# Performance work log

Measured on AMD Instinct MI355X. Metric: run time of the kernel, lower is better.

The kernel has to match this reference:

```python
import jax, jax.numpy as jnp
import numpy as np
import math

B, L, D = 2, 2048, 1024
H, HD = 16, 64          # num heads, head dim
R = 256                 # kv lora rank = D // 4
E, K, F = 8, 2, 1024    # routed experts, top_k, intermediate size


def rmsnorm(x, w, eps=1e-6):
    ms = jnp.mean(x * x, axis=-1, keepdims=True)
    return w * (x * jax.lax.rsqrt(ms + eps))


def setup_inputs() -> dict:
    key = jax.random.key(0)
    ks = jax.random.split(key, 16)
    s = 0.02
    return {
        "x": jax.random.normal(ks[0], (B, L, D), jnp.float32),
        "ln1_w": jnp.ones((D,), jnp.float32),
        "q_w": jax.random.normal(ks[1], (D, H * HD), jnp.float32) * s,
        "kvd_w": jax.random.normal(ks[2], (D, R), jnp.float32) * s,
        "kvn_w": jnp.ones((R,), jnp.float32),
        "kvu_w": jax.random.normal(ks[3], (R, 2 * H * HD), jnp.float32) * s,
        "o_w": jax.random.normal(ks[4], (H * HD, D), jnp.float32) * s,
        "ln2_w": jnp.ones((D,), jnp.float32),
        "gate_w": jax.random.normal(ks[5], (D, E), jnp.float32) * s,
        "sh_w1": jax.random.normal(ks[6], (D, F), jnp.float32) * s,
        "sh_w2": jax.random.normal(ks[7], (F, D), jnp.float32) * s,
        "sh_w3": jax.random.normal(ks[8], (D, F), jnp.float32) * s,
        "re_w1": jax.random.normal(ks[9], (E, D, F), jnp.float32) * s,
        "re_w2": jax.random.normal(ks[10], (E, F, D), jnp.float32) * s,
        "re_w3": jax.random.normal(ks[11], (E, D, F), jnp.float32) * s,
    }


def reference(x, ln1_w, q_w, kvd_w, kvn_w, kvu_w, o_w, ln2_w, gate_w,
              sh_w1, sh_w2, sh_w3, re_w1, re_w2, re_w3):
    # ---- MLHA attention with pre-RMSNorm and latent-compressed KV ----
    xn = rmsnorm(x, ln1_w)
    q = (xn @ q_w).reshape(B, L, H, HD)
    latent = rmsnorm(xn @ kvd_w, kvn_w)                 # [B,L,R]
    kv = latent @ kvu_w                                 # [B,L,2*H*HD]
    k, v = jnp.split(kv, 2, axis=-1)
    k = k.reshape(B, L, H, HD)
    v = v.reshape(B, L, H, HD)
    scores = jnp.einsum('bxhd,byhd->bhxy', q, k) / math.sqrt(HD)
    causal = jnp.tril(jnp.ones((L, L), bool))
    scores = jnp.where(causal, scores, -jnp.inf)
    attn = jax.nn.softmax(scores, axis=-1)
    attn_out = jnp.einsum('bhxy,byhd->bxhd', attn, v).reshape(B, L, H * HD)
    h = x + attn_out @ o_w

    # ---- MoE (inference: no jitter, expert_bias = 0, no bias update) ----
    hn = rmsnorm(h, ln2_w)
    flat = hn.reshape(-1, D)                            # [T,D], T=B*L
    # shared expert (SwiGLU)
    shared = (jax.nn.silu(flat @ sh_w1) * (flat @ sh_w3)) @ sh_w2
    # router
    logits = flat @ gate_w                              # [T,E]
    probs = jax.nn.softmax(logits, axis=-1)
    topw, topi = jax.lax.top_k(probs, K)                # [T,K]
    topw = topw / jnp.sum(topw, axis=-1, keepdims=True)
    # per-token per-expert combine weight [T,E]
    combine = jnp.sum(topw[..., None] * jax.nn.one_hot(topi, E, dtype=flat.dtype), axis=1)
    # all routed experts densely, then masked combine (same math as masked loop)
    h1 = jnp.einsum('td,edf->etf', flat, re_w1)
    h3 = jnp.einsum('td,edf->etf', flat, re_w3)
    eo = jnp.einsum('etf,efd->etd', jax.nn.silu(h1) * h3, re_w2)
    routed = jnp.einsum('te,etd->td', combine, eo)
    moe_out = (shared + routed).reshape(B, L, D)
    return h + moe_out, probs
```

## Files before the change

kernel.cpp:

```cpp
#include <hip/hip_runtime.h>
#include <hip/hip_bf16.h>
#include <cstdint>
#include <cstddef>

typedef unsigned short u16;
typedef unsigned int u32;
typedef __attribute__((ext_vector_type(8))) short bf16x8;
typedef __attribute__((ext_vector_type(4))) float f32x4;

static constexpr int Bb = 2, Ll = 2048, Dd = 1024, Hh = 16, Rr = 256, Ee = 8, Ff = 1024;
static constexpr int Tt = Bb * Ll;
static constexpr float QSCALE = 0.18033688011112042f;

__device__ __forceinline__ u16 f2bf(float f){
  union { float f; u32 u; } v; v.f = f;
  u32 u = v.u;
  u32 r = u + 0x7FFFu + ((u >> 16) & 1u);
  return (u16)(r >> 16);
}
__device__ __forceinline__ float bf2f(u16 b){
  union { u32 u; float f; } v; v.u = ((u32)b) << 16; return v.f;
}

#define GLDS(gp, lp) __builtin_amdgcn_global_load_lds( \
    (const __attribute__((address_space(1))) unsigned int*)(gp), \
    (__attribute__((address_space(3))) unsigned int*)(lp), 16, 0, 0)

__global__ void transpose5(const float* __restrict__ q_w, const float* __restrict__ o_w,
                           const float* __restrict__ w1, const float* __restrict__ w3,
                           const float* __restrict__ w2,
                           u16* __restrict__ qkvdT, u16* __restrict__ oT,
                           u16* __restrict__ sh13T, u16* __restrict__ sh2T){
  const float* s; u16* d; int off, str;
  switch (blockIdx.z){
    case 0: s = q_w; d = qkvdT; off = 0; str = 1; break;
    case 1: s = o_w; d = oT;    off = 0; str = 1; break;
    case 2: s = w1;  d = sh13T; off = 0; str = 2; break;
    case 3: s = w3;  d = sh13T; off = 1; str = 2; break;
    default: s = w2; d = sh2T;  off = 0; str = 1; break;
  }
  __shared__ float tile[32][33];
  int bx = blockIdx.x * 32, by = blockIdx.y * 32;
  int tx = threadIdx.x, ty = threadIdx.y;
  #pragma unroll
  for (int i = ty; i < 32; i += 8) tile[i][tx] = s[(size_t)(by + i) * 1024 + bx + tx];
  __syncthreads();
  #pragma unroll
  for (int i = ty; i < 32; i += 8)
    d[(size_t)(off + (bx + i) * str) * 1024 + by + tx] = f2bf(tile[tx][i]);
}

__global__ void transposeEx(const float* __restrict__ re_w1, const float* __restrict__ re_w3,
                            const float* __restrict__ re_w2,
                            u16* __restrict__ re13T, u16* __restrict__ re2T){
  int z = blockIdx.z, which = z >> 3, e = z & 7;
  const float* s; u16* d; int off, str;
  size_t eo = (size_t)e * 1024 * 1024;
  if (which == 0){ s = re_w1 + eo; d = re13T + (size_t)e * 2048 * 1024; off = 0; str = 2; }
  else if (which == 1){ s = re_w3 + eo; d = re13T + (size_t)e * 2048 * 1024; off = 1; str = 2; }
  else { s = re_w2 + eo; d = re2T + (size_t)e * 1024 * 1024; off = 0; str = 1; }
  __shared__ float tile[32][33];
  int bx = blockIdx.x * 32, by = blockIdx.y * 32;
  int tx = threadIdx.x, ty = threadIdx.y;
  #pragma unroll
  for (int i = ty; i < 32; i += 8) tile[i][tx] = s[(size_t)(by + i) * 1024 + bx + tx];
  __syncthreads();
  #pragma unroll
  for (int i = ty; i < 32; i += 8)
    d[(size_t)(off + (bx + i) * str) * 1024 + by + tx] = f2bf(tile[tx][i]);
}

__global__ void transpose_conv(const float* __restrict__ src, u16* __restrict__ dst,
                               int K, int N, int dstOff){
  __shared__ float tile[32][33];
  int bx = blockIdx.x * 32, by = blockIdx.y * 32;
  int tx = threadIdx.x, ty = threadIdx.y;
  #pragma unroll
  for (int i = ty; i < 32; i += 8) tile[i][tx] = src[(size_t)(by + i) * N + bx + tx];
  __syncthreads();
  #pragma unroll
  for (int i = ty; i < 32; i += 8)
    dst[(size_t)(dstOff + bx + i) * K + by + tx] = f2bf(tile[tx][i]);
}

template<int DIM>
__global__ void rmsnorm_kernel(const float* __restrict__ x, const float* __restrict__ w,
                               u16* __restrict__ out){
  int t = blockIdx.x;
  const float* xr = x + (size_t)t * DIM;
  u16* orow = out + (size_t)t * DIM;
  int tid = threadIdx.x;
  constexpr int NT = 256;
  constexpr int PER = DIM / NT > 0 ? DIM / NT : 1;
  float vals[PER];
  float ss = 0.f;
  #pragma unroll
  for (int i = 0; i < PER; i++){
    int d = tid + i * NT;
    float v = (d < DIM) ? xr[d] : 0.f;
    vals[i] = v; ss += v * v;
  }
  __shared__ float red[4];
  for (int m = 32; m; m >>= 1) ss += __shfl_xor(ss, m, 64);
  if ((tid & 63) == 0) red[tid >> 6] = ss;
  __syncthreads();
  float tot = red[0] + red[1] + red[2] + red[3];
  float rn = rsqrtf(tot / DIM + 1e-6f);
  #pragma unroll
  for (int i = 0; i < PER; i++){
    int d = tid + i * NT;
    if (d < DIM) orow[d] = f2bf(vals[i] * rn * w[d]);
  }
}

__global__ void router_kernel(const float* __restrict__ h, const float* __restrict__ ln2w,
                              const float* __restrict__ gate,
                              float* __restrict__ probs_out,
                              int* __restrict__ topi, float* __restrict__ topw,
                              u16* __restrict__ hn){
  int t = blockIdx.x; int tid = threadIdx.x;
  const float* hr = h + (size_t)t * Dd;
  float v[4]; float ss = 0.f;
  #pragma unroll
  for (int i = 0; i < 4; i++){ float x = hr[tid + i * 256]; v[i] = x; ss += x * x; }
  __shared__ float red[4];
  for (int m = 32; m; m >>= 1) ss += __shfl_xor(ss, m, 64);
  if ((tid & 63) == 0) red[tid >> 6] = ss;
  __syncthreads();
  float rn = rsqrtf((red[0] + red[1] + red[2] + red[3]) / Dd + 1e-6f);
  float p[8];
  #pragma unroll
  for (int e = 0; e < 8; e++) p[e] = 0.f;
  #pragma unroll
  for (int i = 0; i < 4; i++){
    int d = tid + i * 256;
    float hv = v[i] * rn * ln2w[d];
    hn[(size_t)t * Dd + d] = f2bf(hv);
    const float* g = gate + (size_t)d * 8;
    #pragma unroll
    for (int e = 0; e < 8; e++) p[e] += hv * g[e];
  }
  #pragma unroll
  for (int e = 0; e < 8; e++){
    float x = p[e];
    for (int m = 32; m; m >>= 1) x += __shfl_xor(x, m, 64);
    p[e] = x;
  }
  __shared__ float pe[4][8];
  if ((tid & 63) == 0){ for (int e = 0; e < 8; e++) pe[tid >> 6][e] = p[e]; }
  __syncthreads();
  if (tid == 0){
    float lg[8];
    for (int e = 0; e < 8; e++) lg[e] = pe[0][e] + pe[1][e] + pe[2][e] + pe[3][e];
    float mx = lg[0];
    for (int e = 1; e < 8; e++) mx = fmaxf(mx, lg[e]);
    float pr[8]; float s = 0.f;
    for (int e = 0; e < 8; e++){ pr[e] = __expf(lg[e] - mx); s += pr[e]; }
    float inv = 1.f / s;
    for (int e = 0; e < 8; e++) probs_out[(size_t)t * 8 + e] = pr[e] * inv;
    int i0 = 0;
    for (int e = 1; e < 8; e++) if (pr[e] > pr[i0]) i0 = e;
    int i1 = -1;
    for (int e = 0; e < 8; e++){ if (e == i0) continue; if (i1 < 0 || pr[e] > pr[i1]) i1 = e; }
    float w0 = pr[i0], w1 = pr[i1]; float wn = 1.f / (w0 + w1);
    topi[t * 2] = i0; topi[t * 2 + 1] = i1;
    topw[t * 2] = w0 * wn; topw[t * 2 + 1] = w1 * wn;
  }
}

__global__ void hist_kernel(const int* __restrict__ topi, int* __restrict__ counts){
  __shared__ int h[8];
  int tid = threadIdx.x;
  if (tid < 8) h[tid] = 0;
  __syncthreads();
  int base = blockIdx.x * 512;
  for (int i = tid; i < 512; i += 256) atomicAdd(&h[topi[base + i]], 1);
  __syncthreads();
  if (tid < 8) atomicAdd(&counts[tid], h[tid]);
}

__global__ void bucket_kernel(const int* __restrict__ topi, const float* __restrict__ topw,
                              const int* __restrict__ counts, int* __restrict__ cur,
                              int* __restrict__ entries, float* __restrict__ ew){
  __shared__ int lh[8], lbase[8], lcur[8], loffs[8];
  int tid = threadIdx.x;
  if (tid < 8) lh[tid] = 0;
  __syncthreads();
  int t = blockIdx.x * 256 + tid;
  int e0 = topi[t * 2], e1 = topi[t * 2 + 1];
  atomicAdd(&lh[e0], 1); atomicAdd(&lh[e1], 1);
  __syncthreads();
  if (tid == 0){
    int c = 0;
    for (int e = 0; e < 8; e++){ loffs[e] = c; c += counts[e]; }
  }
  if (tid < 8){ lbase[tid] = atomicAdd(&cur[tid], lh[tid]); lcur[tid] = 0; }
  __syncthreads();
  int p0 = atomicAdd(&lcur[e0], 1);
  int pos0 = loffs[e0] + lbase[e0] + p0;
  entries[pos0] = t; ew[pos0] = topw[t * 2];
  int p1 = atomicAdd(&lcur[e1], 1);
  int pos1 = loffs[e1] + lbase[e1] + p1;
  entries[pos1] = t; ew[pos1] = topw[t * 2 + 1];
}

template<int TM, int ROWMODE, int MODE>
__launch_bounds__(256)
__global__ void gemm_bt(const u16* __restrict__ A, const u16* __restrict__ Bt,
                        void* __restrict__ C, const float* __restrict__ res,
                        int M, int N, int K, int lda, int ldc,
                        const int* __restrict__ entries, const float* __restrict__ ew,
                        const int* __restrict__ counts,
                        float* __restrict__ outAt){
  constexpr int MTC = TM / 32;
  __shared__ __align__(16) u16 As[TM * 32];
  __shared__ __align__(16) u16 Bs[128 * 32];
  __shared__ int els[TM];
  __shared__ float ewl[TM];

  int e = (ROWMODE ? blockIdx.z : 0);
  const u16* Bte = Bt + (size_t)e * N * K;
  int cnt, off;
  if (ROWMODE == 0){ cnt = M; off = 0; }
  else {
    cnt = counts[e];
    off = 0;
    for (int i = 0; i < e; i++) off += counts[i];
  }
  int rt = blockIdx.y * TM;
  if (rt >= cnt) return;
  int cb = blockIdx.x * 128;
  int tid = threadIdx.x;

  if (ROWMODE >= 1){
    if (tid < TM){
      int r = rt + tid;
      els[tid] = (r < cnt) ? entries[off + r] : 0;
      ewl[tid] = (MODE == 4 && r < cnt) ? ew[off + r] : 0.f;
    }
    __syncthreads();
  }

  int sr = tid >> 2;
  int skc = (tid & 3) * 8;
  int rr0 = rt + sr, rr1 = rt + sr + 64;
  size_t ar0 = 0, ar1 = 0;
  if (ROWMODE == 0){ ar0 = (size_t)rr0; ar1 = (size_t)rr1; }
  else if (ROWMODE == 1){ ar0 = (size_t)els[sr];
                          ar1 = (TM == 128) ? (size_t)els[sr + 64] : 0; }
  else {
    int c0 = rr0 < cnt ? rr0 : (cnt - 1);
    int c1 = rr1 < cnt ? rr1 : (cnt - 1);
    ar0 = (size_t)off + c0; ar1 = (size_t)off + c1;
  }
  const u16* pa0 = A + ar0 * lda + skc;
  const u16* pa1 = A + ar1 * lda + skc;
  const u16* pb0 = Bte + (size_t)(cb + sr) * K + skc;
  const u16* pb1 = Bte + (size_t)(cb + sr + 64) * K + skc;
  u16* lA0 = &As[tid * 8];
  u16* lA1 = &As[(TM == 128 ? 2048 : 0) + tid * 8];
  u16* lB0 = &Bs[tid * 8];
  u16* lB1 = &Bs[2048 + tid * 8];

  int w = tid >> 6, lane = tid & 63;
  int wm = w >> 1, wn = w & 1;
  int quad = lane >> 4, l16 = lane & 15;

  f32x4 acc[MTC][4];
  const f32x4 zf = {0.f, 0.f, 0.f, 0.f};
  #pragma unroll
  for (int i = 0; i < MTC; i++)
    #pragma unroll
    for (int j = 0; j < 4; j++) acc[i][j] = zf;

  for (int k0 = 0; k0 < K; k0 += 32){
    __syncthreads();
    GLDS(pa0 + k0, lA0);
    if (TM == 128) GLDS(pa1 + k0, lA1);
    GLDS(pb0 + k0, lB0);
    GLDS(pb1 + k0, lB1);
    __syncthreads();
    bf16x8 af[MTC], bfr[4];
    #pragma unroll
    for (int mt = 0; mt < MTC; mt++)
      af[mt] = *(const bf16x8*)&As[(wm * (TM / 2) + mt * 16 + l16) * 32 + quad * 8];
    #pragma unroll
    for (int nt = 0; nt < 4; nt++)
      bfr[nt] = *(const bf16x8*)&Bs[(wn * 64 + nt * 16 + l16) * 32 + quad * 8];
    #pragma unroll
    for (int mt = 0; mt < MTC; mt++)
      #pragma unroll
      for (int nt = 0; nt < 4; nt++)
        acc[mt][nt] = __builtin_amdgcn_mfma_f32_16x16x32_bf16(af[mt], bfr[nt], acc[mt][nt], 0, 0, 0);
  }

  #pragma unroll
  for (int mt = 0; mt < MTC; mt++){
    #pragma unroll
    for (int nt = 0; nt < 4; nt++){
      #pragma unroll
      for (int r = 0; r < 4; r++){
        int row = wm * (TM / 2) + mt * 16 + quad * 4 + r;
        int col = cb + wn * 64 + nt * 16 + l16;
        int rr = rt + row;
        float v = acc[mt][nt][r];
        if (MODE == 6){
          float pv = __shfl_xor(v, 1, 64);
          if (rr < cnt && (l16 & 1) == 0){
            float sl = v / (1.f + __expf(-v));
            size_t crow = (size_t)((ROWMODE == 1) ? (off + rr) : rr);
            ((u16*)C)[crow * ldc + (col >> 1)] = f2bf(sl * pv);
          }
          continue;
        }
        if (rr >= cnt) continue;
        if (MODE == 0){
          size_t ci = (size_t)((ROWMODE == 1) ? (off + rr) : rr) * ldc + col;
          ((u16*)C)[ci] = f2bf(v);
        } else if (MODE == 1){
          size_t ci = (size_t)rr * ldc + col;
          ((float*)C)[ci] = v + res[ci];
        } else if (MODE == 5){
          if (col < 1024) ((u16*)C)[(size_t)rr * 1024 + col] = f2bf(v * QSCALE);
          else            outAt[(size_t)rr * 256 + (col - 1024)] = v;
        } else {
          int tok = els[row];
          atomicAdd(&outAt[(size_t)tok * ldc + col], ewl[row] * v);
        }
      }
    }
  }
}

#define RBAR() __builtin_amdgcn_s_barrier()
#define SBAR0() __builtin_amdgcn_sched_barrier(0)
#define VMCNT8() do{ asm volatile("s_waitcnt vmcnt(8)" ::: "memory"); \
                     __builtin_amdgcn_sched_barrier(0); }while(0)
#define VMCNT0() do{ asm volatile("s_waitcnt vmcnt(0)" ::: "memory"); \
                     __builtin_amdgcn_sched_barrier(0); }while(0)
#define MMQ(MQ, NQ, FA, FB) do{ \
  _Pragma("unroll") \
  for (int m4_ = 0; m4_ < 4; m4_++){ \
    _Pragma("unroll") \
    for (int n2_ = 0; n2_ < 2; n2_++){ \
      acc[(MQ)*4+m4_][(NQ)*2+n2_] = __builtin_amdgcn_mfma_f32_16x16x32_bf16(FA[m4_][0], FB[n2_][0], acc[(MQ)*4+m4_][(NQ)*2+n2_], 0, 0, 0); \
      acc[(MQ)*4+m4_][(NQ)*2+n2_] = __builtin_amdgcn_mfma_f32_16x16x32_bf16(FA[m4_][1], FB[n2_][1], acc[(MQ)*4+m4_][(NQ)*2+n2_], 0, 0, 0); \
    } \
  } }while(0)
#define RDA(DST, BB, MQ) do{ \
  _Pragma("unroll") \
  for (int m4_ = 0; m4_ < 4; m4_++){ \
    const char* p_ = (const char*)(&As[BB][0]) + (size_t)(wm*128 + (MQ)*64 + m4_*16 + l16)*128; \
    DST[m4_][0] = *(const bf16x8*)(p_ + offk0); \
    DST[m4_][1] = *(const bf16x8*)(p_ + offk1); \
  } }while(0)
#define RDB(DST, BB, NQ) do{ \
  _Pragma("unroll") \
  for (int n2_ = 0; n2_ < 2; n2_++){ \
    const char* p_ = (const char*)(&Bs[BB][0]) + (size_t)(wn*64 + (NQ)*32 + n2_*16 + l16)*128; \
    DST[n2_][0] = *(const bf16x8*)(p_ + offk0); \
    DST[n2_][1] = *(const bf16x8*)(p_ + offk1); \
  } }while(0)
#define STGA(SB, H, KT) do{ \
  GLDS(gA[(H)*2+0] + (size_t)(KT)*64, &As[SB][((H)*128 +  0)*64] + (size_t)tid*8); \
  GLDS(gA[(H)*2+1] + (size_t)(KT)*64, &As[SB][((H)*128 + 64)*64] + (size_t)tid*8); }while(0)
#define STGB(SB, H, KT) do{ \
  GLDS(gB[(H)*2+0] + (size_t)(KT)*64, &Bs[SB][((H)*128 +  0)*64] + (size_t)tid*8); \
  GLDS(gB[(H)*2+1] + (size_t)(KT)*64, &Bs[SB][((H)*128 + 64)*64] + (size_t)tid*8); }while(0)

__launch_bounds__(512, 2)
__global__ void gemm256_up(const u16* __restrict__ A,
                           const u16* __restrict__ sh13, const u16* __restrict__ re13,
                           u16* __restrict__ shg, u16* __restrict__ gr,
                           const int* __restrict__ entries, const int* __restrict__ counts){
  __shared__ __align__(16) u16 As[2][256 * 64];
  __shared__ __align__(16) u16 Bs[2][256 * 64];

  int e = blockIdx.z;
  int cnt, off = 0;
  if (e < 8){
    cnt = counts[e];
    for (int i = 0; i < e; i++) off += counts[i];
  } else cnt = Tt;
  int rt = blockIdx.y * 256;
  if (rt >= cnt) return;
  int cb = blockIdx.x * 256;
  const u16* Bte = (e < 8) ? (re13 + (size_t)e * 2048 * 1024) : sh13;
  u16* Cb = (e < 8) ? gr : shg;

  int tid = threadIdx.x;
  int w = tid >> 6, lane = tid & 63, quad = lane >> 4, l16 = lane & 15;
  int wm = w >> 2, wn = w & 3;
  int swz = (l16 & 7) << 4;
  int offk0 = (quad * 16) ^ swz;
  int offk1 = (64 + quad * 16) ^ swz;

  int trow = tid >> 3;
  int sk = ((((tid & 7) << 4) ^ ((trow & 7) << 4)) >> 1);
  const u16* gA[4]; const u16* gB[4];
  #pragma unroll
  for (int i = 0; i < 4; i++){
    int r = i * 64 + trow;
    int garow;
    if (e < 8){
      int idx = rt + r; if (idx >= cnt) idx = cnt - 1;
      garow = entries[off + idx];
    } else garow = rt + r;
    gA[i] = A + (size_t)garow * 1024 + sk;
    gB[i] = Bte + (size_t)(cb + r) * 1024 + sk;
  }

  f32x4 acc[8][4];
  const f32x4 zf = {0.f, 0.f, 0.f, 0.f};
  #pragma unroll
  for (int i = 0; i < 8; i++)
    #pragma unroll
    for (int j = 0; j < 4; j++) acc[i][j] = zf;

  auto tile = [&](int b, int t2, int mode){
    bf16x8 fa0[4][2], fa1[4][2], fb0[2][2], fb1[2][2];
    RDA(fa0, b, 0); RDB(fb0, b, 0);
    RDB(fb1, b, 1); RDA(fa1, b, 1);
    __builtin_amdgcn_s_setprio(1);
    MMQ(0, 0, fa0, fb0); MMQ(0, 1, fa0, fb1);
    MMQ(1, 0, fa1, fb0); MMQ(1, 1, fa1, fb1);
    __builtin_amdgcn_s_setprio(0);
    if (mode == 2) return;
    SBAR0();
    RBAR();
    if (mode == 0){
      STGB(b, 0, t2); STGB(b, 1, t2); STGA(b, 0, t2); STGA(b, 1, t2);
      VMCNT8();
    } else {
      VMCNT0();
    }
    RBAR();
    SBAR0();
  };

  STGB(0, 0, 0); STGB(0, 1, 0); STGA(0, 0, 0); STGA(0, 1, 0);
  STGB(1, 0, 1); STGB(1, 1, 1); STGA(1, 0, 1); STGA(1, 1, 1);
  VMCNT8();
  RBAR();

  for (int t = 0; t < 14; ++t) tile(t & 1, t + 2, 0);
  tile(0, 0, 1);
  tile(1, 0, 2);

  #pragma unroll
  for (int mi = 0; mi < 8; mi++){
    #pragma unroll
    for (int ni = 0; ni < 4; ni++){
      #pragma unroll
      for (int r = 0; r < 4; r++){
        int row = wm * 128 + (mi >> 2) * 64 + (mi & 3) * 16 + quad * 4 + r;
        int col = cb + wn * 64 + (ni >> 1) * 32 + (ni & 1) * 16 + l16;
        float v = acc[mi][ni][r];
        float pv = __shfl_xor(v, 1, 64);
        int grow = rt + row;
        if (grow < cnt && (l16 & 1) == 0){
          float sl = v / (1.f + __expf(-v));
          size_t crow = (e < 8) ? (size_t)(off + grow) : (size_t)grow;
          Cb[crow * 1024 + (col >> 1)] = f2bf(sl * pv);
        }
      }
    }
  }
}

__global__ void vt_kernel(const u16* __restrict__ kv, u16* __restrict__ vt){
  __shared__ __align__(16) u16 t[64 * 72];
  int kt = blockIdx.x * 64, h = blockIdx.y, b = blockIdx.z;
  size_t bL = (size_t)b * Ll;
  int tid = threadIdx.x;
  int r = tid >> 2, c0 = (tid & 3) * 16;
  const u16* src = kv + (bL + kt + r) * 2048 + 1024 + h * 64 + c0;
  *(uint4*)&t[r * 72 + c0]     = *(const uint4*)(src);
  *(uint4*)&t[r * 72 + c0 + 8] = *(const uint4*)(src + 8);
  __syncthreads();
  int d = tid >> 2; int k0 = (tid & 3) * 16;
  u16 tmp[16];
  #pragma unroll
  for (int j = 0; j < 16; j++) tmp[j] = t[(k0 + j) * 72 + d];
  u16* dst = vt + ((size_t)(b * Hh + h) * 64 + d) * (size_t)Ll + kt + k0;
  *(uint4*)dst       = *(const uint4*)&tmp[0];
  *(uint4*)(dst + 8) = *(const uint4*)&tmp[8];
}

__launch_bounds__(256)
__global__ void attn_kernel(const u16* __restrict__ q, const u16* __restrict__ kv,
                            const u16* __restrict__ vt, u16* __restrict__ out){
  constexpr int LD = 72;
  __shared__ __align__(16) u16 Ks[2][64 * LD];
  __shared__ __align__(16) u16 Vs[2][64 * LD];
  __shared__ __align__(16) u16 Ps[64 * LD];
  int h = blockIdx.y, b = blockIdx.z;
  size_t bL = (size_t)b * Ll;
  int tid = threadIdx.x, w = tid >> 6, lane = tid & 63, quad = lane >> 4, l16 = lane & 15;
  int sr = tid >> 2, sc = (tid & 3) * 16;
  const u16* kbase = kv + (bL + sr) * 2048 + h * 64 + sc;
  const u16* vbase = vt + ((size_t)(b * Hh + h) * 64 + sr) * (size_t)Ll + sc;
  const f32x4 zf = {0.f, 0.f, 0.f, 0.f};

  #pragma unroll
  for (int pass = 0; pass < 2; pass++){
    int q0 = (pass ? (31 - (int)blockIdx.x) : (int)blockIdx.x) * 64;
    int qrow = q0 + w * 16 + l16;

    bf16x8 qf[2];
    #pragma unroll
    for (int ks = 0; ks < 2; ks++)
      qf[ks] = *(const bf16x8*)(q + (bL + qrow) * 1024 + h * 64 + ks * 32 + quad * 8);

    f32x4 oacc[4];
    #pragma unroll
    for (int dt = 0; dt < 4; dt++) oacc[dt] = zf;
    float mprev = -1e30f, lsum = 0.f;

    uint4 kr0 = *(const uint4*)(kbase);
    uint4 kr1 = *(const uint4*)(kbase + 8);
    uint4 vr0 = *(const uint4*)(vbase);
    uint4 vr1 = *(const uint4*)(vbase + 8);
    *(uint4*)&Ks[0][sr * LD + sc]     = kr0;
    *(uint4*)&Ks[0][sr * LD + sc + 8] = kr1;
    *(uint4*)&Vs[0][sr * LD + sc]     = vr0;
    *(uint4*)&Vs[0][sr * LD + sc + 8] = vr1;
    int cur = 0;
    __syncthreads();

    for (int kt = 0; kt <= q0; kt += 64){
      bool pfetch = (kt + 64 <= q0);
      if (pfetch){
        const u16* kp = kbase + (size_t)(kt + 64) * 2048;
        kr0 = *(const uint4*)(kp);
        kr1 = *(const uint4*)(kp + 8);
        const u16* vp = vbase + kt + 64;
        vr0 = *(const uint4*)(vp);
        vr1 = *(const uint4*)(vp + 8);
      }
      const u16* ksp = Ks[cur];
      const u16* vsp = Vs[cur];

      f32x4 sacc[4];
      #pragma unroll
      for (int mt = 0; mt < 4; mt++) sacc[mt] = zf;
      __builtin_amdgcn_s_setprio(1);
      #pragma unroll
      for (int ks = 0; ks < 2; ks++){
        #pragma unroll
        for (int mt = 0; mt < 4; mt++){
          bf16x8 kf = *(const bf16x8*)&ksp[(mt * 16 + l16) * LD + ks * 32 + quad * 8];
          sacc[mt] = __builtin_amdgcn_mfma_f32_16x16x32_bf16(kf, qf[ks], sacc[mt], 0, 0, 0);
        }
      }
      __builtin_amdgcn_s_setprio(0);

      bool diag = (kt == q0);
      int lq = w * 16 + l16;
      float sv[16]; float mx = -1e30f;
      #pragma unroll
      for (int mt = 0; mt < 4; mt++){
        #pragma unroll
        for (int r = 0; r < 4; r++){
          float s = sacc[mt][r];
          if (diag && (mt * 16 + quad * 4 + r > lq)) s = -1e30f;
          sv[mt * 4 + r] = s;
          mx = fmaxf(mx, s);
        }
      }
      mx = fmaxf(mx, __shfl_xor(mx, 16, 64));
      mx = fmaxf(mx, __shfl_xor(mx, 32, 64));
      if (!__all(mx <= mprev)){
        float mnew = fmaxf(mprev, mx);
        float alpha = exp2f(mprev - mnew);
        mprev = mnew;
        lsum *= alpha;
        #pragma unroll
        for (int dt = 0; dt < 4; dt++) oacc[dt] *= alpha;
      }
      float rs = 0.f;
      #pragma unroll
      for (int mt = 0; mt < 4; mt++){
        float p0 = exp2f(sv[mt * 4 + 0] - mprev);
        float p1 = exp2f(sv[mt * 4 + 1] - mprev);
        float p2 = exp2f(sv[mt * 4 + 2] - mprev);
        float p3 = exp2f(sv[mt * 4 + 3] - mprev);
        rs += p0 + p1 + p2 + p3;
        union { uint2 u; __hip_bfloat162 h2[2]; } pk;
        pk.h2[0] = __float22bfloat162_rn(make_float2(p0, p1));
        pk.h2[1] = __float22bfloat162_rn(make_float2(p2, p3));
        *(uint2*)&Ps[(w * 16 + l16) * LD + mt * 16 + quad * 4] = pk.u;
      }
      rs += __shfl_xor(rs, 16, 64);
      rs += __shfl_xor(rs, 32, 64);
      lsum += rs;

      __builtin_amdgcn_s_setprio(1);
      #pragma unroll
      for (int ks = 0; ks < 2; ks++){
        bf16x8 pfr = *(const bf16x8*)&Ps[(w * 16 + l16) * LD + ks * 32 + quad * 8];
        #pragma unroll
        for (int dt = 0; dt < 4; dt++){
          bf16x8 vf = *(const bf16x8*)&vsp[(dt * 16 + l16) * LD + ks * 32 + quad * 8];
          oacc[dt] = __builtin_amdgcn_mfma_f32_16x16x32_bf16(vf, pfr, oacc[dt], 0, 0, 0);
        }
      }
      __builtin_amdgcn_s_setprio(0);

      if (pfetch){
        int nb = cur ^ 1;
        *(uint4*)&Ks[nb][sr * LD + sc]     = kr0;
        *(uint4*)&Ks[nb][sr * LD + sc + 8] = kr1;
        *(uint4*)&Vs[nb][sr * LD + sc]     = vr0;
        *(uint4*)&Vs[nb][sr * LD + sc + 8] = vr1;
        cur = nb;
      }
      __syncthreads();
    }

    float inv = 1.f / lsum;
    #pragma unroll
    for (int dt = 0; dt < 4; dt++){
      union { uint2 u; __hip_bfloat162 h2[2]; } ov;
      ov.h2[0] = __float22bfloat162_rn(make_float2(oacc[dt][0] * inv, oacc[dt][1] * inv));
      ov.h2[1] = __float22bfloat162_rn(make_float2(oacc[dt][2] * inv, oacc[dt][3] * inv));
      *(uint2*)(out + (bL + qrow) * 1024 + h * 64 + dt * 16 + quad * 4) = ov.u;
    }
  }
}

extern "C" void kernel_launch(void* const* d_in, const int* in_sizes, int n_in,
                              void* d_out, int out_size, void* d_ws, size_t ws_size,
                              hipStream_t stream){
  const float* x     = (const float*)d_in[0];
  const float* ln1_w = (const float*)d_in[1];
  const float* q_w   = (const float*)d_in[2];
  const float* kvd_w = (const float*)d_in[3];
  const float* kvn_w = (const float*)d_in[4];
  const float* kvu_w = (const float*)d_in[5];
  const float* o_w   = (const float*)d_in[6];
  const float* ln2_w = (const float*)d_in[7];
  const float* gate_w= (const float*)d_in[8];
  const float* sh_w1 = (const float*)d_in[9];
  const float* sh_w2 = (const float*)d_in[10];
  const float* sh_w3 = (const float*)d_in[11];
  const float* re_w1 = (const float*)d_in[12];
  const float* re_w2 = (const float*)d_in[13];
  const float* re_w3 = (const float*)d_in[14];
  float* out = (float*)d_out;

  char* wp = (char*)d_ws;
  auto alloc = [&](size_t bytes)->char*{
    char* p = wp; wp += (bytes + 255) & ~(size_t)255; return p;
  };
  u16* qkvdT = (u16*)alloc((size_t)1280 * 1024 * 2);
  u16* kvuT  = (u16*)alloc((size_t)2048 * 256 * 2);
  u16* oT    = (u16*)alloc((size_t)1024 * 1024 * 2);
  u16* sh13T = (u16*)alloc((size_t)2048 * 1024 * 2);
  u16* sh2T  = (u16*)alloc((size_t)1024 * 1024 * 2);
  u16* re13T = (u16*)alloc((size_t)8 * 2048 * 1024 * 2);
  u16* re2T  = (u16*)alloc((size_t)8 * 1024 * 1024 * 2);
  u16* xn    = (u16*)alloc((size_t)Tt * 1024 * 2);
  u16* qbuf  = (u16*)alloc((size_t)Tt * 1024 * 2);
  float* latpre = (float*)alloc((size_t)Tt * 256 * 4);
  u16* lat   = (u16*)alloc((size_t)Tt * 256 * 2);
  u16* kvbuf = (u16*)alloc((size_t)Tt * 2048 * 2);
  u16* attnb = (u16*)alloc((size_t)Tt * 1024 * 2);
  float* hbuf = (float*)alloc((size_t)Tt * 1024 * 4);
  u16* vtb   = (u16*)alloc((size_t)Bb * Hh * 64 * Ll * 2);
  u16* gr    = (u16*)alloc((size_t)Tt * 2 * 1024 * 2);
  int* counts = (int*)alloc(32);
  int* cur    = (int*)alloc(32);
  int* topi   = (int*)alloc((size_t)Tt * 2 * 4);
  float* topw = (float*)alloc((size_t)Tt * 2 * 4);
  int* entries= (int*)alloc((size_t)Tt * 2 * 4);
  float* ewt  = (float*)alloc((size_t)Tt * 2 * 4);
  (void)ws_size; (void)n_in; (void)in_sizes; (void)out_size;

  hipMemsetAsync(counts, 0, 32, stream);
  hipMemsetAsync(cur, 0, 32, stream);

  dim3 tb(32, 8);
  transpose5<<<dim3(32, 32, 5), tb, 0, stream>>>(q_w, o_w, sh_w1, sh_w3, sh_w2,
                                                 qkvdT, oT, sh13T, sh2T);
  transpose_conv<<<dim3(8, 32, 1), tb, 0, stream>>>(kvd_w, qkvdT, 1024, 256, 1024);
  transpose_conv<<<dim3(64, 8, 1), tb, 0, stream>>>(kvu_w, kvuT, 256, 2048, 0);
  transposeEx<<<dim3(32, 32, 24), tb, 0, stream>>>(re_w1, re_w3, re_w2, re13T, re2T);

  rmsnorm_kernel<1024><<<Tt, 256, 0, stream>>>(x, ln1_w, xn);

  gemm_bt<64,0,5><<<dim3(10, 64), 256, 0, stream>>>(xn, qkvdT, qbuf, nullptr,
      Tt, 1280, 1024, 1024, 1024, nullptr, nullptr, nullptr, latpre);
  rmsnorm_kernel<256><<<Tt, 256, 0, stream>>>(latpre, kvn_w, lat);
  gemm_bt<128,0,0><<<dim3(16, 32), 256, 0, stream>>>(lat, kvuT, kvbuf, nullptr,
      Tt, 2048, 256, 256, 2048, nullptr, nullptr, nullptr, nullptr);
  vt_kernel<<<dim3(32, 16, 2), 256, 0, stream>>>(kvbuf, vtb);
  attn_kernel<<<dim3(16, 16, 2), 256, 0, stream>>>(qbuf, kvbuf, vtb, attnb);
  gemm_bt<64,0,1><<<dim3(8, 64), 256, 0, stream>>>(attnb, oT, hbuf, x,
      Tt, 1024, 1024, 1024, 1024, nullptr, nullptr, nullptr, nullptr);
  router_kernel<<<Tt, 256, 0, stream>>>(hbuf, ln2_w, gate_w, out + (size_t)Tt * Dd,
                                        topi, topw, xn);
  hist_kernel<<<16, 256, 0, stream>>>(topi, counts);
  bucket_kernel<<<16, 256, 0, stream>>>(topi, topw, counts, cur, entries, ewt);

  gemm256_up<<<dim3(8, 16, 9), 512, 0, stream>>>(xn, sh13T, re13T, kvbuf, gr,
                                                 entries, counts);

  gemm_bt<64,0,1><<<dim3(8, 64), 256, 0, stream>>>(kvbuf, sh2T, out, hbuf,
      Tt, 1024, 1024, 1024, 1024, nullptr, nullptr, nullptr, nullptr);
  gemm_bt<128,2,4><<<dim3(8, 32, 8), 256, 0, stream>>>(gr, re2T, nullptr, nullptr,
      Tt, 1024, 1024, 1024, 1024, entries, ewt, counts, out);
}
```

Before: 547.1 us.

## Rework 256-tile GEMM k-loop and fuse shared/routed down-projections into one kernel

Replaces the double-buffered tile lambda in gemm256_up with a macro k-loop that interleaves LDS fragment reads, async global-to-LDS stages and MFMA quarters, separated by barriers. It adds gemm256_dn, which runs the shared and routed expert down-projections in one 256x256-tile launch and accumulates both into the output with atomics. The o-projection GEMM now also writes h into the output buffer (new MODE 8) so later atomics can add on top. The q/latent and o-projection GEMMs switch from 64-row to 128-row tiles. The many barriers could stall the pipeline, and the shared expert now uses atomic adds instead of plain stores.

```diff
diff --git a/kernel.cpp b/kernel.cpp
--- a/kernel.cpp
+++ b/kernel.cpp
@@ -320,6 +320,11 @@
         } else if (MODE == 1){
           size_t ci = (size_t)rr * ldc + col;
           ((float*)C)[ci] = v + res[ci];
+        } else if (MODE == 8){
+          size_t ci = (size_t)rr * ldc + col;
+          float hv = v + res[ci];
+          ((float*)C)[ci] = hv;
+          outAt[ci] = hv;
         } else if (MODE == 5){
           if (col < 1024) ((u16*)C)[(size_t)rr * 1024 + col] = f2bf(v * QSCALE);
           else            outAt[(size_t)rr * 256 + (col - 1024)] = v;
@@ -333,11 +338,6 @@
 }
 
 #define RBAR() __builtin_amdgcn_s_barrier()
-#define SBAR0() __builtin_amdgcn_sched_barrier(0)
-#define VMCNT8() do{ asm volatile("s_waitcnt vmcnt(8)" ::: "memory"); \
-                     __builtin_amdgcn_sched_barrier(0); }while(0)
-#define VMCNT0() do{ asm volatile("s_waitcnt vmcnt(0)" ::: "memory"); \
-                     __builtin_amdgcn_sched_barrier(0); }while(0)
 #define MMQ(MQ, NQ, FA, FB) do{ \
   _Pragma("unroll") \
   for (int m4_ = 0; m4_ < 4; m4_++){ \
@@ -368,6 +368,54 @@
   GLDS(gB[(H)*2+0] + (size_t)(KT)*64, &Bs[SB][((H)*128 +  0)*64] + (size_t)tid*8); \
   GLDS(gB[(H)*2+1] + (size_t)(KT)*64, &Bs[SB][((H)*128 + 64)*64] + (size_t)tid*8); }while(0)
 
+#define GEMM256_KLOOP() do{ \
+  STGB(0, 0, 0); STGB(0, 1, 0); \
+  STGA(0, 0, 0); STGA(0, 1, 0); \
+  __syncthreads(); \
+  bf16x8 fa0[4][2], fa1[4][2], fb0[2][2], fb1[2][2]; \
+  for (int it = 0; it < 8; ++it){ \
+    int t1 = 2 * it + 1, t2 = 2 * it + 2; \
+    RDA(fa0, 0, 0); RDB(fb0, 0, 0); \
+    STGB(1, 0, t1); \
+    RBAR(); \
+    __builtin_amdgcn_s_setprio(1); MMQ(0, 0, fa0, fb0); __builtin_amdgcn_s_setprio(0); \
+    RBAR(); \
+    RDB(fb1, 0, 1); \
+    STGB(1, 1, t1); \
+    RBAR(); \
+    __builtin_amdgcn_s_setprio(1); MMQ(0, 1, fa0, fb1); __builtin_amdgcn_s_setprio(0); \
+    RBAR(); \
+    RDA(fa1, 0, 1); \
+    STGA(1, 0, t1); \
+    RBAR(); \
+    __builtin_amdgcn_s_setprio(1); MMQ(1, 0, fa1, fb0); __builtin_amdgcn_s_setprio(0); \
+    RBAR(); \
+    STGA(1, 1, t1); \
+    RBAR(); \
+    __builtin_amdgcn_s_setprio(1); MMQ(1, 1, fa1, fb1); __builtin_amdgcn_s_setprio(0); \
+    __syncthreads(); \
+    bool pf = (it < 7); \
+    RDA(fa0, 1, 0); RDB(fb0, 1, 0); \
+    if (pf) STGB(0, 0, t2); \
+    RBAR(); \
+    __builtin_amdgcn_s_setprio(1); MMQ(0, 0, fa0, fb0); __builtin_amdgcn_s_setprio(0); \
+    RBAR(); \
+    RDB(fb1, 1, 1); \
+    if (pf) STGB(0, 1, t2); \
+    RBAR(); \
+    __builtin_amdgcn_s_setprio(1); MMQ(0, 1, fa0, fb1); __builtin_amdgcn_s_setprio(0); \
+    RBAR(); \
+    RDA(fa1, 1, 1); \
+    if (pf) STGA(0, 0, t2); \
+    RBAR(); \
+    __builtin_amdgcn_s_setprio(1); MMQ(1, 0, fa1, fb0); __builtin_amdgcn_s_setprio(0); \
+    RBAR(); \
+    if (pf) STGA(0, 1, t2); \
+    RBAR(); \
+    __builtin_amdgcn_s_setprio(1); MMQ(1, 1, fa1, fb1); __builtin_amdgcn_s_setprio(0); \
+    __syncthreads(); \
+  } }while(0)
+
 __launch_bounds__(512, 2)
 __global__ void gemm256_up(const u16* __restrict__ A,
                            const u16* __restrict__ sh13, const u16* __restrict__ re13,
@@ -417,35 +465,7 @@
     #pragma unroll
     for (int j = 0; j < 4; j++) acc[i][j] = zf;
 
-  auto tile = [&](int b, int t2, int mode){
-    bf16x8 fa0[4][2], fa1[4][2], fb0[2][2], fb1[2][2];
-    RDA(fa0, b, 0); RDB(fb0, b, 0);
-    RDB(fb1, b, 1); RDA(fa1, b, 1);
-    __builtin_amdgcn_s_setprio(1);
-    MMQ(0, 0, fa0, fb0); MMQ(0, 1, fa0, fb1);
-    MMQ(1, 0, fa1, fb0); MMQ(1, 1, fa1, fb1);
-    __builtin_amdgcn_s_setprio(0);
-    if (mode == 2) return;
-    SBAR0();
-    RBAR();
-    if (mode == 0){
-      STGB(b, 0, t2); STGB(b, 1, t2); STGA(b, 0, t2); STGA(b, 1, t2);
-      VMCNT8();
-    } else {
-      VMCNT0();
-    }
-    RBAR();
-    SBAR0();
-  };
-
-  STGB(0, 0, 0); STGB(0, 1, 0); STGA(0, 0, 0); STGA(0, 1, 0);
-  STGB(1, 0, 1); STGB(1, 1, 1); STGA(1, 0, 1); STGA(1, 1, 1);
-  VMCNT8();
-  RBAR();
-
-  for (int t = 0; t < 14; ++t) tile(t & 1, t + 2, 0);
-  tile(0, 0, 1);
-  tile(1, 0, 2);
+  GEMM256_KLOOP();
 
   #pragma unroll
   for (int mi = 0; mi < 8; mi++){
@@ -462,6 +482,91 @@
           float sl = v / (1.f + __expf(-v));
           size_t crow = (e < 8) ? (size_t)(off + grow) : (size_t)grow;
           Cb[crow * 1024 + (col >> 1)] = f2bf(sl * pv);
+        }
+      }
+    }
+  }
+}
+
+__launch_bounds__(512, 2)
+__global__ void gemm256_dn(const u16* __restrict__ Agr, const u16* __restrict__ Ash,
+                           const u16* __restrict__ sh2, const u16* __restrict__ re2,
+                           float* __restrict__ outp,
+                           const int* __restrict__ entries, const float* __restrict__ ew,
+                           const int* __restrict__ counts){
+  __shared__ __align__(16) u16 As[2][256 * 64];
+  __shared__ __align__(16) u16 Bs[2][256 * 64];
+  __shared__ int els[256];
+  __shared__ float ewl[256];
+
+  int e = blockIdx.z;
+  int cnt, off = 0;
+  if (e < 8){
+    cnt = counts[e];
+    for (int i = 0; i < e; i++) off += counts[i];
+  } else cnt = Tt;
+  int rt = blockIdx.y * 256;
+  if (rt >= cnt) return;
+  int cb = blockIdx.x * 256;
+  const u16* Bte = (e < 8) ? (re2 + (size_t)e * 1024 * 1024) : sh2;
+
+  int tid = threadIdx.x;
+  int w = tid >> 6, lane = tid & 63, quad = lane >> 4, l16 = lane & 15;
+  int wm = w >> 2, wn = w & 3;
+  int swz = (l16 & 7) << 4;
+  int offk0 = (quad * 16) ^ swz;
+  int offk1 = (64 + quad * 16) ^ swz;
+
+  if (e < 8 && tid < 256){
+    int i = rt + tid; if (i >= cnt) i = cnt - 1;
+    int idx = off + i; if (idx > Tt * 2 - 1) idx = Tt * 2 - 1;
+    els[tid] = entries[idx];
+    ewl[tid] = ew[idx];
+  }
+
+  int trow = tid >> 3;
+  int sk = ((((tid & 7) << 4) ^ ((trow & 7) << 4)) >> 1);
+  const u16* gA[4]; const u16* gB[4];
+  #pragma unroll
+  for (int i = 0; i < 4; i++){
+    int r = i * 64 + trow;
+    size_t arow;
+    if (e < 8){
+      int idx = rt + r; if (idx >= cnt) idx = cnt - 1;
+      arow = (size_t)(off + idx);
+      gA[i] = Agr + arow * 1024 + sk;
+    } else {
+      gA[i] = Ash + (size_t)(rt + r) * 1024 + sk;
+    }
+    gB[i] = Bte + (size_t)(cb + r) * 1024 + sk;
+  }
+
+  f32x4 acc[8][4];
+  const f32x4 zf = {0.f, 0.f, 0.f, 0.f};
+  #pragma unroll
+  for (int i = 0; i < 8; i++)
+    #pragma unroll
+    for (int j = 0; j < 4; j++) acc[i][j] = zf;
+
+  GEMM256_KLOOP();
+
+  #pragma unroll
+  for (int mi = 0; mi < 8; mi++){
+    #pragma unroll
+    for (int ni = 0; ni < 4; ni++){
+      #pragma unroll
+      for (int r = 0; r < 4; r++){
+        int row = wm * 128 + (mi >> 2) * 64 + (mi & 3) * 16 + quad * 4 + r;
+        int col = cb + wn * 64 + (ni >> 1) * 32 + (ni & 1) * 16 + l16;
+        int grow = rt + row;
+        if (grow < cnt){
+          float v = acc[mi][ni][r];
+          if (e < 8){
+            int tok = els[row];
+            atomicAdd(&outp[(size_t)tok * 1024 + col], ewl[row] * v);
+          } else {
+            atomicAdd(&outp[(size_t)grow * 1024 + col], v);
+          }
         }
       }
     }
@@ -689,15 +794,15 @@
 
   rmsnorm_kernel<1024><<<Tt, 256, 0, stream>>>(x, ln1_w, xn);
 
-  gemm_bt<64,0,5><<<dim3(10, 64), 256, 0, stream>>>(xn, qkvdT, qbuf, nullptr,
+  gemm_bt<128,0,5><<<dim3(10, 32), 256, 0, stream>>>(xn, qkvdT, qbuf, nullptr,
       Tt, 1280, 1024, 1024, 1024, nullptr, nullptr, nullptr, latpre);
   rmsnorm_kernel<256><<<Tt, 256, 0, stream>>>(latpre, kvn_w, lat);
   gemm_bt<128,0,0><<<dim3(16, 32), 256, 0, stream>>>(lat, kvuT, kvbuf, nullptr,
       Tt, 2048, 256, 256, 2048, nullptr, nullptr, nullptr, nullptr);
   vt_kernel<<<dim3(32, 16, 2), 256, 0, stream>>>(kvbuf, vtb);
   attn_kernel<<<dim3(16, 16, 2), 256, 0, stream>>>(qbuf, kvbuf, vtb, attnb);
-  gemm_bt<64,0,1><<<dim3(8, 64), 256, 0, stream>>>(attnb, oT, hbuf, x,
-      Tt, 1024, 1024, 1024, 1024, nullptr, nullptr, nullptr, nullptr);
+  gemm_bt<128,0,8><<<dim3(8, 32), 256, 0, stream>>>(attnb, oT, hbuf, x,
+      Tt, 1024, 1024, 1024, 1024, nullptr, nullptr, nullptr, out);
   router_kernel<<<Tt, 256, 0, stream>>>(hbuf, ln2_w, gate_w, out + (size_t)Tt * Dd,
                                         topi, topw, xn);
   hist_kernel<<<16, 256, 0, stream>>>(topi, counts);
@@ -706,8 +811,6 @@
   gemm256_up<<<dim3(8, 16, 9), 512, 0, stream>>>(xn, sh13T, re13T, kvbuf, gr,
                                                  entries, counts);
 
-  gemm_bt<64,0,1><<<dim3(8, 64), 256, 0, stream>>>(kvbuf, sh2T, out, hbuf,
-      Tt, 1024, 1024, 1024, 1024, nullptr, nullptr, nullptr, nullptr);
-  gemm_bt<128,2,4><<<dim3(8, 32, 8), 256, 0, stream>>>(gr, re2T, nullptr, nullptr,
-      Tt, 1024, 1024, 1024, 1024, entries, ewt, counts, out);
-}
+  gemm256_dn<<<dim3(4, 16, 9), 512, 0, stream>>>(gr, kvbuf, sh2T, re2T, out,
+                                                 entries, ewt, counts);
+}
```

Result: slower. 577.0 us (+5.5%).
